# Performance work log

Measured on AMD Instinct MI355X. Metric: run time of the kernel, lower is better.

Reference implementation:

```python
import jax, jax.numpy as jnp
import numpy as np

SIGMA0 = 0.001
T = 8
H = 1.0 / T
N, M, D = 4096, 4096, 64


def setup_inputs() -> dict:
    key = jax.random.key(0)
    k1, k2 = jax.random.split(key)
    z = jax.random.normal(k1, (N, D), dtype=jnp.float32)
    x0 = jax.random.normal(k2, (M, D), dtype=jnp.float32)
    return {"z": z, "x0": x0}


def _q_field(t, x, x0):
    # u[n,m] = ||x_n - (1-t)*x0_m||^2 / (2*sigma(t)^2)
    # expanded form avoids materializing the (N, M, D) difference tensor;
    # softmax(-u + umin) == softmax(-u) (shift invariance).
    alphat = 1.0 - t
    sigmat = SIGMA0 + (1.0 - SIGMA0) * t
    x_sq = jnp.sum(x * x, axis=-1)[:, None]          # (N, 1)
    x0_sq = jnp.sum(x0 * x0, axis=-1)[None, :]       # (1, M)
    cross = jnp.einsum('nd,md->nm', x, x0)           # (N, M)
    u = (x_sq - 2.0 * alphat * cross + (alphat * alphat) * x0_sq) / (2.0 * sigmat * sigmat)
    wt = jax.nn.softmax(-u, axis=-1)                 # (N, M)
    return wt @ x0                                   # (N, D)


def _G(t, x, x0):
    qt = _q_field(t, x, x0)
    sigmat = SIGMA0 + (1.0 - SIGMA0) * t
    return ((1.0 - SIGMA0) * x - qt) / sigmat


def reference(z, x0):
    xt = z
    G1 = _G(jnp.float32(1.0), xt, x0)
    # Heun (predictor-corrector) loop: t = (T-i-1)*h for i in 0..T-2
    ts = ((T - jnp.arange(T - 1, dtype=jnp.float32) - 1.0) * H).astype(jnp.float32)

    def step(carry, t):
        xt, G1 = carry
        G2 = _G(t, xt - G1 * H, x0)
        xt = xt - (G1 + G2) * (H / 2.0)
        # torch code does G1 = G2.detach().clone()
        return (xt, jax.lax.stop_gradient(G2)), None

    (xt, _), _ = jax.lax.scan(step, (xt, G1), ts)
    return xt
```

## Files before the change

### kernel.cpp

```cpp
#include <hip/hip_runtime.h>
#include <hip/hip_bf16.h>

typedef short  short8  __attribute__((ext_vector_type(8)));
typedef float  float4v __attribute__((ext_vector_type(4)));
typedef uint   uint4v  __attribute__((ext_vector_type(4)));

#define N_ROWS 4096
#define DDIM   64
#define NKB    (N_ROWS / 64)
#define NSPLIT 16
#define NT4    (NKB / NSPLIT)
#define HSTEP  0.125f
#define SIG0   0.001f

__device__ __forceinline__ ushort f2bf(float f) {
    __hip_bfloat16 h = __float2bfloat16(f);
    return *reinterpret_cast<ushort*>(&h);
}
__device__ __forceinline__ float bf2f(ushort u) {
    return __uint_as_float(((unsigned)u) << 16);
}
__device__ __forceinline__ float4v mfma16(short8 a, short8 b, float4v c) {
    return __builtin_amdgcn_mfma_f32_16x16x32_bf16(a, b, c, 0, 0, 0);
}

__global__ __launch_bounds__(256) void x0stats_kernel(
    const float* __restrict__ x0, float* __restrict__ x0sq,
    float* __restrict__ x0sum)
{
    __shared__ float cs[64];
    const int tid = threadIdx.x;
    if (tid < 64) cs[tid] = 0.f;
    __syncthreads();
    const int r  = blockIdx.x * 64 + (tid >> 2);
    const int c0 = (tid & 3) * 16;
    const float4* rp = (const float4*)(x0 + (size_t)r * DDIM + c0);
    float f[16];
    float ss = 0.f;
#pragma unroll
    for (int k = 0; k < 4; ++k) {
        float4 v = rp[k];
        f[4 * k] = v.x; f[4 * k + 1] = v.y; f[4 * k + 2] = v.z; f[4 * k + 3] = v.w;
        ss += v.x * v.x + v.y * v.y + v.z * v.z + v.w * v.w;
    }
    ss += __shfl_xor(ss, 1, 64);
    ss += __shfl_xor(ss, 2, 64);
    if ((tid & 3) == 0) x0sq[r] = ss;
#pragma unroll
    for (int j = 0; j < 16; ++j) atomicAdd(&cs[c0 + j], f[j]);
    __syncthreads();
    if (tid < 64) atomicAdd(&x0sum[tid], cs[tid]);
}

__global__ __launch_bounds__(256) void prep_pack_kernel(
    const float* __restrict__ x0,
    short8* __restrict__ Apk_h, short8* __restrict__ Apk_l,
    short8* __restrict__ Bpk_h, short8* __restrict__ Bpk_l)
{
    __shared__ float xt_[64][65];
    const int tid  = threadIdx.x;
    const int kb64 = blockIdx.x;
    {
        const int r = tid >> 2, c0 = (tid & 3) * 16;
        const float4* src = (const float4*)(x0 + ((size_t)(kb64 * 64 + r)) * DDIM + c0);
#pragma unroll
        for (int k = 0; k < 4; ++k) {
            float4 v = src[k];
            xt_[r][c0 + 4 * k + 0] = v.x; xt_[r][c0 + 4 * k + 1] = v.y;
            xt_[r][c0 + 4 * k + 2] = v.z; xt_[r][c0 + 4 * k + 3] = v.w;
        }
    }
    __syncthreads();
    const int w = tid >> 6, lane = tid & 63, qi = lane & 15, g = lane >> 4;
#pragma unroll
    for (int half = 0; half < 2; ++half) {
        short8 h, l;
#pragma unroll
        for (int j = 0; j < 8; ++j) {
            float v = xt_[w * 16 + qi][half * 32 + g * 8 + j];
            ushort hh = f2bf(v);
            h[j] = (short)hh;
            l[j] = (short)f2bf(v - bf2f(hh));
        }
        size_t idx = (((size_t)kb64 * 4 + w) * 2 + half) * 64 + lane;
        Apk_h[idx] = h; Apk_l[idx] = l;
    }
#pragma unroll
    for (int pp = 0; pp < 2; ++pp) {
        int pw = w + pp * 4;
        int ks2 = pw >> 2, dsub = pw & 3;
        short8 h, l;
#pragma unroll
        for (int j = 0; j < 8; ++j) {
            float v = xt_[ks2 * 32 + g * 8 + j][dsub * 16 + qi];
            ushort hh = f2bf(v);
            h[j] = (short)hh;
            l[j] = (short)f2bf(v - bf2f(hh));
        }
        size_t idx = (((size_t)kb64 * 2 + ks2) * 4 + dsub) * 64 + lane;
        Bpk_h[idx] = h; Bpk_l[idx] = l;
    }
}

__global__ __launch_bounds__(256) void g1_init_kernel(
    const float* __restrict__ z, const float* __restrict__ x0sum,
    float* __restrict__ G1)
{
    int i = blockIdx.x * 256 + threadIdx.x;
    G1[i] = (1.0f - SIG0) * z[i] - x0sum[i & 63] * (1.0f / 4096.0f);
}

__global__ __launch_bounds__(1024) void g_full_kernel(
    float* __restrict__ xt, const float* __restrict__ G1, float c2,
    const short8* __restrict__ Apk_h, const short8* __restrict__ Apk_l,
    const short8* __restrict__ Bpk_h, const short8* __restrict__ Bpk_l,
    const float* __restrict__ x0sq, float scale, float beta,
    float inv_sig, float* __restrict__ G2out)
{
    __shared__ float part[NSPLIT][16][65];
    __shared__ float m_lds[NSPLIT][17];
    __shared__ float l_lds[NSPLIT][17];

    const int tid  = threadIdx.x;
    const int w    = tid >> 6;
    const int lane = tid & 63;
    const int g    = lane >> 4;
    const int qi   = lane & 15;
    const int row  = blockIdx.x * 16 + qi;

    short8 xbh[2], xbl[2];
    {
        const float* a = xt + (size_t)row * DDIM;
        const float* b = G1 + (size_t)row * DDIM;
#pragma unroll
        for (int ds_ = 0; ds_ < 2; ++ds_) {
            const int d0 = ds_ * 32 + g * 8;
#pragma unroll
            for (int j = 0; j < 8; ++j) {
                float x = a[d0 + j] + c2 * b[d0 + j];
                ushort h = f2bf(x);
                xbh[ds_][j] = (short)h;
                xbl[ds_][j] = (short)f2bf(x - bf2f(h));
            }
        }
    }

    float4v pvacc[4];
#pragma unroll
    for (int d = 0; d < 4; ++d) pvacc[d] = (float4v){0.f, 0.f, 0.f, 0.f};
    float m = -1.0e30f, lsum = 0.f;

    for (int tile = 0; tile < NT4; ++tile) {
        const int kbi = w * NT4 + tile;
        const int kb  = kbi * 64;

        float sc[4][4];
#pragma unroll
        for (int ks = 0; ks < 4; ++ks) {
            const size_t ai = (((size_t)kbi * 4 + ks) * 2) * 64 + lane;
            short8 Ah0 = Apk_h[ai];
            short8 Ah1 = Apk_h[ai + 64];
            short8 Al0 = Apk_l[ai];
            short8 Al1 = Apk_l[ai + 64];
            float4v acc = (float4v){0.f, 0.f, 0.f, 0.f};
            __builtin_amdgcn_s_setprio(1);
            acc = mfma16(Ah0, xbh[0], acc);
            acc = mfma16(Ah1, xbh[1], acc);
            acc = mfma16(Al0, xbh[0], acc);
            acc = mfma16(Al1, xbh[1], acc);
            acc = mfma16(Ah0, xbl[0], acc);
            acc = mfma16(Ah1, xbl[1], acc);
            __builtin_amdgcn_s_setprio(0);
            const float4 sq = *(const float4*)(x0sq + kb + ks * 16 + g * 4);
            sc[ks][0] = scale * acc[0] - beta * sq.x;
            sc[ks][1] = scale * acc[1] - beta * sq.y;
            sc[ks][2] = scale * acc[2] - beta * sq.z;
            sc[ks][3] = scale * acc[3] - beta * sq.w;
        }

        float tmax = sc[0][0];
#pragma unroll
        for (int ks = 0; ks < 4; ++ks)
#pragma unroll
            for (int r = 0; r < 4; ++r) tmax = fmaxf(tmax, sc[ks][r]);
        tmax = fmaxf(tmax, __shfl_xor(tmax, 16, 64));
        tmax = fmaxf(tmax, __shfl_xor(tmax, 32, 64));
        const float mn = fmaxf(m, tmax);
        const float co = __expf(m - mn);
        float psum = 0.f;
#pragma unroll
        for (int ks = 0; ks < 4; ++ks)
#pragma unroll
            for (int r = 0; r < 4; ++r) {
                sc[ks][r] = __expf(sc[ks][r] - mn);
                psum += sc[ks][r];
            }
        psum += __shfl_xor(psum, 16, 64);
        psum += __shfl_xor(psum, 32, 64);
        lsum = lsum * co + psum;
        m = mn;
        float co_r[4];
#pragma unroll
        for (int r = 0; r < 4; ++r) co_r[r] = __shfl(co, g * 4 + r, 64);
#pragma unroll
        for (int d = 0; d < 4; ++d)
#pragma unroll
            for (int r = 0; r < 4; ++r) pvacc[d][r] *= co_r[r];

        uint pkh[4][2], pkl[4][2];
#pragma unroll
        for (int ks = 0; ks < 4; ++ks)
#pragma unroll
            for (int pr = 0; pr < 2; ++pr) {
                float f0 = sc[ks][2 * pr], f1 = sc[ks][2 * pr + 1];
                ushort h0 = f2bf(f0), h1 = f2bf(f1);
                pkh[ks][pr] = (uint)h0 | ((uint)h1 << 16);
                ushort e0 = f2bf(f0 - bf2f(h0)), e1 = f2bf(f1 - bf2f(h1));
                pkl[ks][pr] = (uint)e0 | ((uint)e1 << 16);
            }

#pragma unroll
        for (int ks2 = 0; ks2 < 2; ++ks2) {
            uint4v pah, pal;
#pragma unroll
            for (int c = 0; c < 4; ++c) {
                const int src = (2 * (g & 1) + (c >> 1)) * 16 + qi;
                uint h0 = (uint)__shfl((int)pkh[2 * ks2][c & 1], src, 64);
                uint h1 = (uint)__shfl((int)pkh[2 * ks2 + 1][c & 1], src, 64);
                pah[c] = (g >= 2) ? h1 : h0;
                uint l0 = (uint)__shfl((int)pkl[2 * ks2][c & 1], src, 64);
                uint l1 = (uint)__shfl((int)pkl[2 * ks2 + 1][c & 1], src, 64);
                pal[c] = (g >= 2) ? l1 : l0;
            }
            const short8 PAh = __builtin_bit_cast(short8, pah);
            const short8 PAl = __builtin_bit_cast(short8, pal);
#pragma unroll
            for (int dsub = 0; dsub < 4; ++dsub) {
                const size_t bi = (((size_t)kbi * 2 + ks2) * 4 + dsub) * 64 + lane;
                short8 Bh = Bpk_h[bi];
                short8 Bl = Bpk_l[bi];
                __builtin_amdgcn_s_setprio(1);
                pvacc[dsub] = mfma16(PAh, Bh, pvacc[dsub]);
                pvacc[dsub] = mfma16(PAh, Bl, pvacc[dsub]);
                pvacc[dsub] = mfma16(PAl, Bh, pvacc[dsub]);
                __builtin_amdgcn_s_setprio(0);
            }
        }
    }

#pragma unroll
    for (int dsub = 0; dsub < 4; ++dsub)
#pragma unroll
        for (int r = 0; r < 4; ++r)
            part[w][g * 4 + r][dsub * 16 + qi] = pvacc[dsub][r];
    if (g == 0) { m_lds[w][qi] = m; l_lds[w][qi] = lsum; }
    __syncthreads();

    {
        const int crow = tid >> 6;
        const int d    = tid & 63;
        float mstar = m_lds[0][crow];
#pragma unroll
        for (int i = 1; i < NSPLIT; ++i) mstar = fmaxf(mstar, m_lds[i][crow]);
        float L = 0.f, num = 0.f;
#pragma unroll
        for (int i = 0; i < NSPLIT; ++i) {
            float e = __expf(m_lds[i][crow] - mstar);
            L   += l_lds[i][crow] * e;
            num += part[i][crow][d] * e;
        }
        const float qt = num / L;
        const size_t idx = ((size_t)blockIdx.x * 16 + crow) * DDIM + d;
        const float g1v = G1[idx];
        const float xv  = xt[idx] + c2 * g1v;
        const float g2  = ((1.0f - SIG0) * xv - qt) * inv_sig;
        G2out[idx] = g2;
        xt[idx] -= (g1v + g2) * (HSTEP * 0.5f);
    }
}

extern "C" void kernel_launch(void* const* d_in, const int* in_sizes, int n_in,
                              void* d_out, int out_size, void* d_ws, size_t ws_size,
                              hipStream_t stream) {
    const float* z  = (const float*)d_in[0];
    const float* x0 = (const float*)d_in[1];
    float* xt = (float*)d_out;

    char* p = (char*)d_ws;
    auto alloc = [&](size_t bytes) {
        char* q = p; p += (bytes + 255) & ~(size_t)255; return q;
    };
    float*  G1    = (float*)alloc((size_t)N_ROWS * DDIM * 4);
    float*  G2    = (float*)alloc((size_t)N_ROWS * DDIM * 4);
    float*  x0sq  = (float*)alloc((size_t)N_ROWS * 4);
    float*  x0sum = (float*)alloc(64 * 4);
    short8* Apk_h = (short8*)alloc((size_t)NKB * 4 * 2 * 64 * 16);
    short8* Apk_l = (short8*)alloc((size_t)NKB * 4 * 2 * 64 * 16);
    short8* Bpk_h = (short8*)alloc((size_t)NKB * 2 * 4 * 64 * 16);
    short8* Bpk_l = (short8*)alloc((size_t)NKB * 2 * 4 * 64 * 16);

    hipMemcpyAsync(xt, z, (size_t)N_ROWS * DDIM * 4, hipMemcpyDeviceToDevice, stream);
    hipMemsetAsync(x0sum, 0, 64 * 4, stream);
    x0stats_kernel<<<NKB, 256, 0, stream>>>(x0, x0sq, x0sum);
    prep_pack_kernel<<<NKB, 256, 0, stream>>>(x0, Apk_h, Apk_l, Bpk_h, Bpk_l);
    g1_init_kernel<<<(N_ROWS * DDIM) / 256, 256, 0, stream>>>(z, x0sum, G1);

    for (int i = 0; i < 7; ++i) {
        float t  = (float)(7 - i) / 8.0f;
        float al = 1.0f - t;
        float sg = SIG0 + (1.0f - SIG0) * t;
        float scale = al / (sg * sg);
        float beta  = al * al / (2.0f * sg * sg);
        g_full_kernel<<<N_ROWS / 16, 1024, 0, stream>>>(
            xt, G1, -HSTEP, Apk_h, Apk_l, Bpk_h, Bpk_l, x0sq, scale, beta,
            1.0f / sg, G2);
        float* tmp = G1; G1 = G2; G2 = tmp;
    }
}
```

Before: 256.0 us.

## Fuse all seven Heun steps into one persistent kernel with LDS-resident state

Merges the x0 statistics pass into the pack kernel, and folds the G1 init plus all seven per-step kernels into one flow_kernel. Each 16-row block keeps xt and G1 in shared memory across steps and writes the output once at the end. This removes the device memcpy, several kernel launches and the per-step global round trips of xt and G1/G2. The per-row work is unchanged, and shared memory per block grows slightly.

```diff
diff --git a/kernel.cpp b/kernel.cpp
--- a/kernel.cpp
+++ b/kernel.cpp
@@ -24,53 +24,40 @@
     return __builtin_amdgcn_mfma_f32_16x16x32_bf16(a, b, c, 0, 0, 0);
 }
 
-__global__ __launch_bounds__(256) void x0stats_kernel(
-    const float* __restrict__ x0, float* __restrict__ x0sq,
-    float* __restrict__ x0sum)
-{
-    __shared__ float cs[64];
-    const int tid = threadIdx.x;
-    if (tid < 64) cs[tid] = 0.f;
-    __syncthreads();
-    const int r  = blockIdx.x * 64 + (tid >> 2);
-    const int c0 = (tid & 3) * 16;
-    const float4* rp = (const float4*)(x0 + (size_t)r * DDIM + c0);
-    float f[16];
-    float ss = 0.f;
-#pragma unroll
-    for (int k = 0; k < 4; ++k) {
-        float4 v = rp[k];
-        f[4 * k] = v.x; f[4 * k + 1] = v.y; f[4 * k + 2] = v.z; f[4 * k + 3] = v.w;
-        ss += v.x * v.x + v.y * v.y + v.z * v.z + v.w * v.w;
-    }
-    ss += __shfl_xor(ss, 1, 64);
-    ss += __shfl_xor(ss, 2, 64);
-    if ((tid & 3) == 0) x0sq[r] = ss;
-#pragma unroll
-    for (int j = 0; j < 16; ++j) atomicAdd(&cs[c0 + j], f[j]);
-    __syncthreads();
-    if (tid < 64) atomicAdd(&x0sum[tid], cs[tid]);
-}
-
 __global__ __launch_bounds__(256) void prep_pack_kernel(
     const float* __restrict__ x0,
     short8* __restrict__ Apk_h, short8* __restrict__ Apk_l,
-    short8* __restrict__ Bpk_h, short8* __restrict__ Bpk_l)
+    short8* __restrict__ Bpk_h, short8* __restrict__ Bpk_l,
+    float* __restrict__ x0sq, float* __restrict__ x0sum)
 {
     __shared__ float xt_[64][65];
+    __shared__ float cs[64];
     const int tid  = threadIdx.x;
     const int kb64 = blockIdx.x;
+    if (tid < 64) cs[tid] = 0.f;
+    __syncthreads();
     {
         const int r = tid >> 2, c0 = (tid & 3) * 16;
         const float4* src = (const float4*)(x0 + ((size_t)(kb64 * 64 + r)) * DDIM + c0);
+        float ss = 0.f;
 #pragma unroll
         for (int k = 0; k < 4; ++k) {
             float4 v = src[k];
             xt_[r][c0 + 4 * k + 0] = v.x; xt_[r][c0 + 4 * k + 1] = v.y;
             xt_[r][c0 + 4 * k + 2] = v.z; xt_[r][c0 + 4 * k + 3] = v.w;
-        }
+            ss += v.x * v.x + v.y * v.y + v.z * v.z + v.w * v.w;
+            atomicAdd(&cs[c0 + 4 * k + 0], v.x);
+            atomicAdd(&cs[c0 + 4 * k + 1], v.y);
+            atomicAdd(&cs[c0 + 4 * k + 2], v.z);
+            atomicAdd(&cs[c0 + 4 * k + 3], v.w);
+        }
+        ss += __shfl_xor(ss, 1, 64);
+        ss += __shfl_xor(ss, 2, 64);
+        if ((tid & 3) == 0) x0sq[kb64 * 64 + r] = ss;
     }
     __syncthreads();
+    if (tid < 64) atomicAdd(&x0sum[tid], cs[tid]);
+
     const int w = tid >> 6, lane = tid & 63, qi = lane & 15, g = lane >> 4;
 #pragma unroll
     for (int half = 0; half < 2; ++half) {
@@ -102,22 +89,15 @@
     }
 }
 
-__global__ __launch_bounds__(256) void g1_init_kernel(
+__global__ __launch_bounds__(1024) void flow_kernel(
     const float* __restrict__ z, const float* __restrict__ x0sum,
-    float* __restrict__ G1)
-{
-    int i = blockIdx.x * 256 + threadIdx.x;
-    G1[i] = (1.0f - SIG0) * z[i] - x0sum[i & 63] * (1.0f / 4096.0f);
-}
-
-__global__ __launch_bounds__(1024) void g_full_kernel(
-    float* __restrict__ xt, const float* __restrict__ G1, float c2,
     const short8* __restrict__ Apk_h, const short8* __restrict__ Apk_l,
     const short8* __restrict__ Bpk_h, const short8* __restrict__ Bpk_l,
-    const float* __restrict__ x0sq, float scale, float beta,
-    float inv_sig, float* __restrict__ G2out)
+    const float* __restrict__ x0sq, float* __restrict__ xt_out)
 {
-    __shared__ float part[NSPLIT][16][65];
+    __shared__ float xt_lds[16][65];
+    __shared__ float G1_lds[16][65];
+    __shared__ float part[NSPLIT][16][66];
     __shared__ float m_lds[NSPLIT][17];
     __shared__ float l_lds[NSPLIT][17];
 
@@ -126,157 +106,171 @@
     const int lane = tid & 63;
     const int g    = lane >> 4;
     const int qi   = lane & 15;
-    const int row  = blockIdx.x * 16 + qi;
-
-    short8 xbh[2], xbl[2];
+    const int crow = tid >> 6;
+    const int d    = tid & 63;
+    const int rowbase = blockIdx.x * 16;
+
     {
-        const float* a = xt + (size_t)row * DDIM;
-        const float* b = G1 + (size_t)row * DDIM;
+        float zv = z[(size_t)(rowbase + crow) * DDIM + d];
+        xt_lds[crow][d] = zv;
+        G1_lds[crow][d] = (1.0f - SIG0) * zv - x0sum[d] * (1.0f / 4096.0f);
+    }
+    __syncthreads();
+
+    for (int step = 0; step < 7; ++step) {
+        const float t  = (float)(7 - step) * 0.125f;
+        const float al = 1.0f - t;
+        const float sg = SIG0 + (1.0f - SIG0) * t;
+        const float scale = al / (sg * sg);
+        const float beta  = al * al / (2.0f * sg * sg);
+        const float inv_sig = 1.0f / sg;
+
+        short8 xbh[2], xbl[2];
 #pragma unroll
         for (int ds_ = 0; ds_ < 2; ++ds_) {
             const int d0 = ds_ * 32 + g * 8;
 #pragma unroll
             for (int j = 0; j < 8; ++j) {
-                float x = a[d0 + j] + c2 * b[d0 + j];
+                float x = xt_lds[qi][d0 + j] - HSTEP * G1_lds[qi][d0 + j];
                 ushort h = f2bf(x);
                 xbh[ds_][j] = (short)h;
                 xbl[ds_][j] = (short)f2bf(x - bf2f(h));
             }
         }
-    }
-
-    float4v pvacc[4];
-#pragma unroll
-    for (int d = 0; d < 4; ++d) pvacc[d] = (float4v){0.f, 0.f, 0.f, 0.f};
-    float m = -1.0e30f, lsum = 0.f;
-
-    for (int tile = 0; tile < NT4; ++tile) {
-        const int kbi = w * NT4 + tile;
-        const int kb  = kbi * 64;
-
-        float sc[4][4];
-#pragma unroll
-        for (int ks = 0; ks < 4; ++ks) {
-            const size_t ai = (((size_t)kbi * 4 + ks) * 2) * 64 + lane;
-            short8 Ah0 = Apk_h[ai];
-            short8 Ah1 = Apk_h[ai + 64];
-            short8 Al0 = Apk_l[ai];
-            short8 Al1 = Apk_l[ai + 64];
-            float4v acc = (float4v){0.f, 0.f, 0.f, 0.f};
-            __builtin_amdgcn_s_setprio(1);
-            acc = mfma16(Ah0, xbh[0], acc);
-            acc = mfma16(Ah1, xbh[1], acc);
-            acc = mfma16(Al0, xbh[0], acc);
-            acc = mfma16(Al1, xbh[1], acc);
-            acc = mfma16(Ah0, xbl[0], acc);
-            acc = mfma16(Ah1, xbl[1], acc);
-            __builtin_amdgcn_s_setprio(0);
-            const float4 sq = *(const float4*)(x0sq + kb + ks * 16 + g * 4);
-            sc[ks][0] = scale * acc[0] - beta * sq.x;
-            sc[ks][1] = scale * acc[1] - beta * sq.y;
-            sc[ks][2] = scale * acc[2] - beta * sq.z;
-            sc[ks][3] = scale * acc[3] - beta * sq.w;
-        }
-
-        float tmax = sc[0][0];
-#pragma unroll
-        for (int ks = 0; ks < 4; ++ks)
-#pragma unroll
-            for (int r = 0; r < 4; ++r) tmax = fmaxf(tmax, sc[ks][r]);
-        tmax = fmaxf(tmax, __shfl_xor(tmax, 16, 64));
-        tmax = fmaxf(tmax, __shfl_xor(tmax, 32, 64));
-        const float mn = fmaxf(m, tmax);
-        const float co = __expf(m - mn);
-        float psum = 0.f;
-#pragma unroll
-        for (int ks = 0; ks < 4; ++ks)
-#pragma unroll
-            for (int r = 0; r < 4; ++r) {
-                sc[ks][r] = __expf(sc[ks][r] - mn);
-                psum += sc[ks][r];
-            }
-        psum += __shfl_xor(psum, 16, 64);
-        psum += __shfl_xor(psum, 32, 64);
-        lsum = lsum * co + psum;
-        m = mn;
-        float co_r[4];
-#pragma unroll
-        for (int r = 0; r < 4; ++r) co_r[r] = __shfl(co, g * 4 + r, 64);
-#pragma unroll
-        for (int d = 0; d < 4; ++d)
-#pragma unroll
-            for (int r = 0; r < 4; ++r) pvacc[d][r] *= co_r[r];
-
-        uint pkh[4][2], pkl[4][2];
-#pragma unroll
-        for (int ks = 0; ks < 4; ++ks)
-#pragma unroll
-            for (int pr = 0; pr < 2; ++pr) {
-                float f0 = sc[ks][2 * pr], f1 = sc[ks][2 * pr + 1];
-                ushort h0 = f2bf(f0), h1 = f2bf(f1);
-                pkh[ks][pr] = (uint)h0 | ((uint)h1 << 16);
-                ushort e0 = f2bf(f0 - bf2f(h0)), e1 = f2bf(f1 - bf2f(h1));
-                pkl[ks][pr] = (uint)e0 | ((uint)e1 << 16);
-            }
-
-#pragma unroll
-        for (int ks2 = 0; ks2 < 2; ++ks2) {
-            uint4v pah, pal;
-#pragma unroll
-            for (int c = 0; c < 4; ++c) {
-                const int src = (2 * (g & 1) + (c >> 1)) * 16 + qi;
-                uint h0 = (uint)__shfl((int)pkh[2 * ks2][c & 1], src, 64);
-                uint h1 = (uint)__shfl((int)pkh[2 * ks2 + 1][c & 1], src, 64);
-                pah[c] = (g >= 2) ? h1 : h0;
-                uint l0 = (uint)__shfl((int)pkl[2 * ks2][c & 1], src, 64);
-                uint l1 = (uint)__shfl((int)pkl[2 * ks2 + 1][c & 1], src, 64);
-                pal[c] = (g >= 2) ? l1 : l0;
-            }
-            const short8 PAh = __builtin_bit_cast(short8, pah);
-            const short8 PAl = __builtin_bit_cast(short8, pal);
-#pragma unroll
-            for (int dsub = 0; dsub < 4; ++dsub) {
-                const size_t bi = (((size_t)kbi * 2 + ks2) * 4 + dsub) * 64 + lane;
-                short8 Bh = Bpk_h[bi];
-                short8 Bl = Bpk_l[bi];
+
+        float4v pvacc[4];
+#pragma unroll
+        for (int dd = 0; dd < 4; ++dd) pvacc[dd] = (float4v){0.f, 0.f, 0.f, 0.f};
+        float m = -1.0e30f, lsum = 0.f;
+
+        for (int tile = 0; tile < NT4; ++tile) {
+            const int kbi = w * NT4 + tile;
+            const int kb  = kbi * 64;
+
+            float sc[4][4];
+#pragma unroll
+            for (int ks = 0; ks < 4; ++ks) {
+                const size_t ai = (((size_t)kbi * 4 + ks) * 2) * 64 + lane;
+                short8 Ah0 = Apk_h[ai];
+                short8 Ah1 = Apk_h[ai + 64];
+                short8 Al0 = Apk_l[ai];
+                short8 Al1 = Apk_l[ai + 64];
+                float4v acc = (float4v){0.f, 0.f, 0.f, 0.f};
                 __builtin_amdgcn_s_setprio(1);
-                pvacc[dsub] = mfma16(PAh, Bh, pvacc[dsub]);
-                pvacc[dsub] = mfma16(PAh, Bl, pvacc[dsub]);
-                pvacc[dsub] = mfma16(PAl, Bh, pvacc[dsub]);
+                acc = mfma16(Ah0, xbh[0], acc);
+                acc = mfma16(Ah1, xbh[1], acc);
+                acc = mfma16(Al0, xbh[0], acc);
+                acc = mfma16(Al1, xbh[1], acc);
+                acc = mfma16(Ah0, xbl[0], acc);
+                acc = mfma16(Ah1, xbl[1], acc);
                 __builtin_amdgcn_s_setprio(0);
-            }
-        }
-    }
-
-#pragma unroll
-    for (int dsub = 0; dsub < 4; ++dsub)
-#pragma unroll
-        for (int r = 0; r < 4; ++r)
-            part[w][g * 4 + r][dsub * 16 + qi] = pvacc[dsub][r];
-    if (g == 0) { m_lds[w][qi] = m; l_lds[w][qi] = lsum; }
-    __syncthreads();
-
-    {
-        const int crow = tid >> 6;
-        const int d    = tid & 63;
-        float mstar = m_lds[0][crow];
-#pragma unroll
-        for (int i = 1; i < NSPLIT; ++i) mstar = fmaxf(mstar, m_lds[i][crow]);
-        float L = 0.f, num = 0.f;
-#pragma unroll
-        for (int i = 0; i < NSPLIT; ++i) {
-            float e = __expf(m_lds[i][crow] - mstar);
-            L   += l_lds[i][crow] * e;
-            num += part[i][crow][d] * e;
-        }
-        const float qt = num / L;
-        const size_t idx = ((size_t)blockIdx.x * 16 + crow) * DDIM + d;
-        const float g1v = G1[idx];
-        const float xv  = xt[idx] + c2 * g1v;
-        const float g2  = ((1.0f - SIG0) * xv - qt) * inv_sig;
-        G2out[idx] = g2;
-        xt[idx] -= (g1v + g2) * (HSTEP * 0.5f);
-    }
+                const float4 sq = *(const float4*)(x0sq + kb + ks * 16 + g * 4);
+                sc[ks][0] = scale * acc[0] - beta * sq.x;
+                sc[ks][1] = scale * acc[1] - beta * sq.y;
+                sc[ks][2] = scale * acc[2] - beta * sq.z;
+                sc[ks][3] = scale * acc[3] - beta * sq.w;
+            }
+
+            float tmax = sc[0][0];
+#pragma unroll
+            for (int ks = 0; ks < 4; ++ks)
+#pragma unroll
+                for (int r = 0; r < 4; ++r) tmax = fmaxf(tmax, sc[ks][r]);
+            tmax = fmaxf(tmax, __shfl_xor(tmax, 16, 64));
+            tmax = fmaxf(tmax, __shfl_xor(tmax, 32, 64));
+            const float mn = fmaxf(m, tmax);
+            const float co = __expf(m - mn);
+            float psum = 0.f;
+#pragma unroll
+            for (int ks = 0; ks < 4; ++ks)
+#pragma unroll
+                for (int r = 0; r < 4; ++r) {
+                    sc[ks][r] = __expf(sc[ks][r] - mn);
+                    psum += sc[ks][r];
+                }
+            psum += __shfl_xor(psum, 16, 64);
+            psum += __shfl_xor(psum, 32, 64);
+            lsum = lsum * co + psum;
+            m = mn;
+            float co_r[4];
+#pragma unroll
+            for (int r = 0; r < 4; ++r) co_r[r] = __shfl(co, g * 4 + r, 64);
+#pragma unroll
+            for (int dd = 0; dd < 4; ++dd)
+#pragma unroll
+                for (int r = 0; r < 4; ++r) pvacc[dd][r] *= co_r[r];
+
+            uint pkh[4][2], pkl[4][2];
+#pragma unroll
+            for (int ks = 0; ks < 4; ++ks)
+#pragma unroll
+                for (int pr = 0; pr < 2; ++pr) {
+                    float f0 = sc[ks][2 * pr], f1 = sc[ks][2 * pr + 1];
+                    ushort h0 = f2bf(f0), h1 = f2bf(f1);
+                    pkh[ks][pr] = (uint)h0 | ((uint)h1 << 16);
+                    ushort e0 = f2bf(f0 - bf2f(h0)), e1 = f2bf(f1 - bf2f(h1));
+                    pkl[ks][pr] = (uint)e0 | ((uint)e1 << 16);
+                }
+
+#pragma unroll
+            for (int ks2 = 0; ks2 < 2; ++ks2) {
+                uint4v pah, pal;
+#pragma unroll
+                for (int c = 0; c < 4; ++c) {
+                    const int src = (2 * (g & 1) + (c >> 1)) * 16 + qi;
+                    uint h0 = (uint)__shfl((int)pkh[2 * ks2][c & 1], src, 64);
+                    uint h1 = (uint)__shfl((int)pkh[2 * ks2 + 1][c & 1], src, 64);
+                    pah[c] = (g >= 2) ? h1 : h0;
+                    uint l0 = (uint)__shfl((int)pkl[2 * ks2][c & 1], src, 64);
+                    uint l1 = (uint)__shfl((int)pkl[2 * ks2 + 1][c & 1], src, 64);
+                    pal[c] = (g >= 2) ? l1 : l0;
+                }
+                const short8 PAh = __builtin_bit_cast(short8, pah);
+                const short8 PAl = __builtin_bit_cast(short8, pal);
+#pragma unroll
+                for (int dsub = 0; dsub < 4; ++dsub) {
+                    const size_t bi = (((size_t)kbi * 2 + ks2) * 4 + dsub) * 64 + lane;
+                    short8 Bh = Bpk_h[bi];
+                    short8 Bl = Bpk_l[bi];
+                    __builtin_amdgcn_s_setprio(1);
+                    pvacc[dsub] = mfma16(PAh, Bh, pvacc[dsub]);
+                    pvacc[dsub] = mfma16(PAh, Bl, pvacc[dsub]);
+                    pvacc[dsub] = mfma16(PAl, Bh, pvacc[dsub]);
+                    __builtin_amdgcn_s_setprio(0);
+                }
+            }
+        }
+
+#pragma unroll
+        for (int dsub = 0; dsub < 4; ++dsub)
+#pragma unroll
+            for (int r = 0; r < 4; ++r)
+                part[w][g * 4 + r][dsub * 16 + qi] = pvacc[dsub][r];
+        if (g == 0) { m_lds[w][qi] = m; l_lds[w][qi] = lsum; }
+        __syncthreads();
+
+        {
+            float mstar = m_lds[0][crow];
+#pragma unroll
+            for (int i = 1; i < NSPLIT; ++i) mstar = fmaxf(mstar, m_lds[i][crow]);
+            float L = 0.f, num = 0.f;
+#pragma unroll
+            for (int i = 0; i < NSPLIT; ++i) {
+                float e = __expf(m_lds[i][crow] - mstar);
+                L   += l_lds[i][crow] * e;
+                num += part[i][crow][d] * e;
+            }
+            const float qt  = num / L;
+            const float g1v = G1_lds[crow][d];
+            const float xv  = xt_lds[crow][d] - HSTEP * g1v;
+            const float g2  = ((1.0f - SIG0) * xv - qt) * inv_sig;
+            xt_lds[crow][d] -= (g1v + g2) * (HSTEP * 0.5f);
+            G1_lds[crow][d]  = g2;
+        }
+        __syncthreads();
+    }
+
+    xt_out[(size_t)(rowbase + crow) * DDIM + d] = xt_lds[crow][d];
 }
 
 extern "C" void kernel_launch(void* const* d_in, const int* in_sizes, int n_in,
@@ -290,8 +284,6 @@
     auto alloc = [&](size_t bytes) {
         char* q = p; p += (bytes + 255) & ~(size_t)255; return q;
     };
-    float*  G1    = (float*)alloc((size_t)N_ROWS * DDIM * 4);
-    float*  G2    = (float*)alloc((size_t)N_ROWS * DDIM * 4);
     float*  x0sq  = (float*)alloc((size_t)N_ROWS * 4);
     float*  x0sum = (float*)alloc(64 * 4);
     short8* Apk_h = (short8*)alloc((size_t)NKB * 4 * 2 * 64 * 16);
@@ -299,21 +291,9 @@
     short8* Bpk_h = (short8*)alloc((size_t)NKB * 2 * 4 * 64 * 16);
     short8* Bpk_l = (short8*)alloc((size_t)NKB * 2 * 4 * 64 * 16);
 
-    hipMemcpyAsync(xt, z, (size_t)N_ROWS * DDIM * 4, hipMemcpyDeviceToDevice, stream);
     hipMemsetAsync(x0sum, 0, 64 * 4, stream);
-    x0stats_kernel<<<NKB, 256, 0, stream>>>(x0, x0sq, x0sum);
-    prep_pack_kernel<<<NKB, 256, 0, stream>>>(x0, Apk_h, Apk_l, Bpk_h, Bpk_l);
-    g1_init_kernel<<<(N_ROWS * DDIM) / 256, 256, 0, stream>>>(z, x0sum, G1);
-
-    for (int i = 0; i < 7; ++i) {
-        float t  = (float)(7 - i) / 8.0f;
-        float al = 1.0f - t;
-        float sg = SIG0 + (1.0f - SIG0) * t;
-        float scale = al / (sg * sg);
-        float beta  = al * al / (2.0f * sg * sg);
-        g_full_kernel<<<N_ROWS / 16, 1024, 0, stream>>>(
-            xt, G1, -HSTEP, Apk_h, Apk_l, Bpk_h, Bpk_l, x0sq, scale, beta,
-            1.0f / sg, G2);
-        float* tmp = G1; G1 = G2; G2 = tmp;
-    }
-}
+    prep_pack_kernel<<<NKB, 256, 0, stream>>>(x0, Apk_h, Apk_l, Bpk_h, Bpk_l,
+                                              x0sq, x0sum);
+    flow_kernel<<<N_ROWS / 16, 1024, 0, stream>>>(z, x0sum, Apk_h, Apk_l,
+                                                  Bpk_h, Bpk_l, x0sq, xt);
+}
```

Measured after the change: 212.6 us. -17.0%, faster.
